# Optimization experiments

Measured on AMD Instinct MI355X. Metric: run time of the kernel, lower is better.

## Reference

```python
import jax, jax.numpy as jnp
import numpy as np

E, N, C, A, S, H, HD, RH = 320000, 20000, 128, 4, 16, 8, 32, 64
AH = H * HD  # 256 attn-head channels; mul_alpha = AH, mul_alpha_head = HD
OUT = 128


def smooth_leaky_relu(x, a=0.2):
    # Equiformer SmoothLeakyReLU: 0.5*((1+a)*x + (1-a)*x*(2*sigmoid(x)-1))
    return 0.5 * ((1 + a) * x + (1 - a) * x * (2.0 * jax.nn.sigmoid(x) - 1.0))


def setup_inputs() -> dict:
    key = jax.random.key(0)
    ks = jax.random.split(key, 20)
    d = {
        'message': jax.random.normal(ks[0], (E, C), jnp.float32),
        'edge_attr': jax.random.normal(ks[1], (E, A), jnp.float32),
        'edge_scalars': jax.random.normal(ks[2], (E, S), jnp.float32),
        'w_rad1': jax.random.normal(ks[3], (S, RH), jnp.float32) / np.sqrt(S),
        'b_rad1': jnp.zeros((RH,), jnp.float32),
        'w_rad2': jax.random.normal(ks[4], (RH, C * A), jnp.float32) / np.sqrt(RH),
        'b_rad2': jnp.zeros((C * A,), jnp.float32),
        'w_dtp_v': jax.random.normal(ks[5], (C, A), jnp.float32) / np.sqrt(A),
        'w_lin_act': jax.random.normal(ks[6], (C, C), jnp.float32) / np.sqrt(C),
        'b_lin_act': jnp.zeros((C,), jnp.float32),
        'w_alpha': jax.random.normal(ks[7], (C, AH), jnp.float32) / np.sqrt(C),
        'b_alpha': jnp.zeros((AH,), jnp.float32),
        'w_lin_v': jax.random.normal(ks[8], (C, AH), jnp.float32) / np.sqrt(C),
        'b_lin_v': jnp.zeros((AH,), jnp.float32),
        'alpha_dot': jax.random.normal(ks[9], (H, HD), jnp.float32) / np.sqrt(HD),
        'w_proj': jax.random.normal(ks[10], (AH, OUT), jnp.float32) / np.sqrt(AH),
        'b_proj': jnp.zeros((OUT,), jnp.float32),
        'edge_dst': jax.random.randint(ks[11], (E,), 0, N, jnp.int32),
        'n_nodes_dst': N,
    }
    return d


def reference(message, edge_attr, edge_scalars,
              w_rad1, b_rad1, w_rad2, b_rad2,
              w_dtp_v, w_lin_act, b_lin_act,
              w_alpha, b_alpha, w_lin_v, b_lin_v,
              alpha_dot, w_proj, b_proj,
              edge_dst, n_nodes_dst):
    n = n_nodes_dst
    # dtp_rad: radial MLP -> per-edge depthwise TP weights [E, C, A]
    h = jax.nn.silu(edge_scalars @ w_rad1 + b_rad1)
    w = (h @ w_rad2 + b_rad2).reshape(-1, C, A)
    # sep_act.dtp (scalar irreps): out[e,c] = msg[e,c] * sum_a w[e,c,a]*attr[e,a]
    msg = message * jnp.einsum('eca,ea->ec', w, edge_attr)
    # sep_alpha -> alpha heads [E, H, HD]
    alpha = (msg @ w_alpha + b_alpha).reshape(-1, H, HD)
    # sep_act.lin + gate (scalars -> SiLU)
    value = jax.nn.silu(msg @ w_lin_act + b_lin_act)
    # sep_value: internal-weight dtp then linear, reshape to heads
    value = value * jnp.einsum('ca,ea->ec', w_dtp_v, edge_attr)
    value = (value @ w_lin_v + b_lin_v).reshape(-1, H, HD)
    # attention logits
    alpha = smooth_leaky_relu(alpha)
    alpha = jnp.einsum('ehk,hk->eh', alpha, alpha_dot)
    # scatter softmax over destination nodes
    amax = jax.ops.segment_max(alpha, edge_dst, num_segments=n)  # [N, H]
    amax = jnp.where(jnp.isfinite(amax), amax, 0.0)
    ex = jnp.exp(alpha - amax[edge_dst])
    denom = jax.ops.segment_sum(ex, edge_dst, num_segments=n)
    alpha = ex / (denom[edge_dst] + 1e-16)
    # weighted scatter-add aggregation
    attn = value * alpha[..., None]  # [E, H, HD]
    node = jax.ops.segment_sum(attn, edge_dst, num_segments=n)  # [N, H, HD]
    node = node.reshape(n, AH)  # heads2vec
    return node @ w_proj + b_proj
```

## Files before the change

### kernel.cpp

```cpp
#include <hip/hip_runtime.h>
#include <hip/hip_bf16.h>

#define C_   128
#define A_   4
#define S_   16
#define RH_  64
#define H_   8
#define AH_  256
#define OUT_ 128

typedef __attribute__((ext_vector_type(8))) short bf16x8;
typedef __attribute__((ext_vector_type(4))) float f32x4;

__device__ __forceinline__ float sigf(float x) { return 1.0f / (1.0f + __expf(-x)); }

__device__ __forceinline__ unsigned short f2bf(float x) {
    unsigned u = __float_as_uint(x);
    unsigned r = (u + 0x7fffu + ((u >> 16) & 1u)) >> 16;
    return (unsigned short)r;
}
__device__ __forceinline__ float bf2f(unsigned short v) {
    return __uint_as_float((unsigned)v << 16);
}

__device__ __forceinline__ unsigned pkbf(float a, float b) {
    union { __hip_bfloat162 h; unsigned u; } c;
    c.h = __float22bfloat162_rn(float2{a, b});
    return c.u;
}

__device__ __forceinline__ unsigned enc(float x) {
    unsigned b = __float_as_uint(x);
    return (b & 0x80000000u) ? ~b : (b | 0x80000000u);
}
__device__ __forceinline__ float dec(unsigned u) {
    unsigned b = (u & 0x80000000u) ? (u & 0x7fffffffu) : ~u;
    return __uint_as_float(b);
}

__global__ void k_pack(const float* __restrict__ W, short* __restrict__ out, int K, int N) {
    const int KS = K / 32;
    const int ct = blockIdx.x / KS, ks = blockIdx.x % KS;
    const int l = threadIdx.x, lr = l & 15, lg = l >> 4;
    bf16x8 v;
    #pragma unroll
    for (int j = 0; j < 8; j++)
        v[j] = (short)f2bf(W[(size_t)(ks * 32 + lg * 8 + j) * N + ct * 16 + lr]);
    *(bf16x8*)&out[((size_t)blockIdx.x * 64 + l) * 8] = v;
}

__global__ void k_pack_dtp(const float* __restrict__ W, short* __restrict__ out) {
    const int ct = blockIdx.x >> 3, ks = blockIdx.x & 7;
    const int l = threadIdx.x, lr = l & 15, lg = l >> 4;
    bf16x8 v;
    #pragma unroll
    for (int j = 0; j < 8; j++)
        v[j] = (short)f2bf(W[(size_t)(ks * 8 + lg * 2 + (j >> 2)) * 512 + (ct * 16 + lr) * 4 + (j & 3)]);
    *(bf16x8*)&out[((size_t)blockIdx.x * 64 + l) * 8] = v;
}

__global__ __launch_bounds__(256) void k_hist(
    const int* __restrict__ edge_dst, int* __restrict__ deg, int E)
{
    const int e = blockIdx.x * 256 + threadIdx.x;
    if (e < E) atomicAdd(&deg[edge_dst[e]], 1);
}

__global__ __launch_bounds__(1024) void k_scan(
    const int* __restrict__ deg, int* __restrict__ cursor, int N)
{
    __shared__ int part[1024];
    const int t = threadIdx.x;
    const int per = (N + 1023) / 1024;
    const int i0 = t * per;
    int s = 0;
    for (int i = 0; i < per; i++) { int idx = i0 + i; if (idx < N) s += deg[idx]; }
    part[t] = s;
    __syncthreads();
    for (int off = 1; off < 1024; off <<= 1) {
        int v = (t >= off) ? part[t - off] : 0;
        __syncthreads();
        part[t] += v;
        __syncthreads();
    }
    int excl = (t == 0) ? 0 : part[t - 1];
    for (int i = 0; i < per; i++) {
        int idx = i0 + i;
        if (idx < N) { cursor[idx] = excl; excl += deg[idx]; }
    }
}

__global__ __launch_bounds__(256) void k_fill(
    const int* __restrict__ edge_dst, int* __restrict__ cursor,
    int* __restrict__ sorted, int E)
{
    const int e = blockIdx.x * 256 + threadIdx.x;
    if (e < E) {
        const int pos = atomicAdd(&cursor[edge_dst[e]], 1);
        sorted[pos] = e;
    }
}

__global__ __launch_bounds__(256, 4) void k_msgalpha(
    const float* __restrict__ message, const float* __restrict__ edge_attr,
    const float* __restrict__ edge_scalars,
    const float* __restrict__ w_rad1, const float* __restrict__ b_rad1,
    const short* __restrict__ w_rad2_lin, const float* __restrict__ b_rad2,
    const short* __restrict__ w_alpha_lin, const float* __restrict__ b_alpha,
    const float* __restrict__ alpha_dot, const int* __restrict__ edge_dst,
    short* __restrict__ msg_bf, float* __restrict__ logits, unsigned* __restrict__ amax_u)
{
    __shared__ __align__(16) char smem[25216];
    short* Ap     = (short*)smem;
    short* msg_s  = (short*)(smem + 16384);
    float* w1_s   = (float*)(smem + 16384);
    float* es_s   = (float*)(smem + 16384 + 4096);
    float* attr_s = (float*)(smem + 24576);
    int*   dst_s  = (int*)(smem + 25088);

    const int t = threadIdx.x;
    const long e0 = (long)blockIdx.x * 32;

    *(float4*)&w1_s[t * 4] = *(const float4*)&w_rad1[t * 4];
    if (t < 128) {
        const int r = t >> 2, s4 = (t & 3) * 4;
        *(float4*)&es_s[r * 17 + s4] = *(const float4*)&edge_scalars[(e0 + r) * S_ + s4];
    }
    if (t < 32) {
        *(float4*)&attr_s[t * 4] = *(const float4*)&edge_attr[(e0 + t) * A_];
        dst_s[t] = edge_dst[e0 + t];
    }
    __syncthreads();

    {
        const int r = t & 31, o0 = (t >> 5) * 8;
        float acc[8];
        #pragma unroll
        for (int i = 0; i < 8; i++) acc[i] = b_rad1[o0 + i];
        #pragma unroll
        for (int s = 0; s < S_; s++) {
            const float ev = es_s[r * 17 + s];
            #pragma unroll
            for (int i = 0; i < 8; i++) acc[i] += ev * w1_s[s * 64 + o0 + i];
        }
        float h[8];
        #pragma unroll
        for (int i = 0; i < 8; i++) { const float x = acc[i]; h[i] = x * sigf(x); }
        const float4 a4 = *(const float4*)&attr_s[r * 4];
        char* base = (char*)Ap + r * 512;
        const int sw = (r & 31) << 4;
        #pragma unroll
        for (int c = 0; c < 4; c++) {
            const float h0 = h[2 * c], h1 = h[2 * c + 1];
            uint4 v;
            v.x = pkbf(h0 * a4.x, h0 * a4.y);
            v.y = pkbf(h0 * a4.z, h0 * a4.w);
            v.z = pkbf(h1 * a4.x, h1 * a4.y);
            v.w = pkbf(h1 * a4.z, h1 * a4.w);
            *(uint4*)(base + ((o0 * 8 + c * 16) ^ sw)) = v;
        }
    }
    __syncthreads();

    const int w = t >> 6, l = t & 63, lr = l & 15, lg = l >> 4;

    {
        #pragma unroll
        for (int q = 0; q < 2; q++) {
            const int ct = w * 2 + q;
            bf16x8 bf[8];
            #pragma unroll
            for (int ks = 0; ks < 8; ks++)
                bf[ks] = *(const bf16x8*)&w_rad2_lin[((size_t)(ct * 8 + ks) * 64 + l) * 8];
            const int col = ct * 16 + lr;
            const float4 b2 = *(const float4*)&b_rad2[col * 4];
            #pragma unroll
            for (int rt = 0; rt < 2; rt++) {
                const int arow = rt * 16 + lr;
                const char* abase = (char*)Ap + arow * 512;
                const int asw = (arow & 31) << 4;
                bf16x8 af[8];
                #pragma unroll
                for (int ks = 0; ks < 8; ks++)
                    af[ks] = *(const bf16x8*)(abase + ((ks * 64 + lg * 16) ^ asw));
                f32x4 acc = {0.f, 0.f, 0.f, 0.f};
                #pragma unroll
                for (int ks = 0; ks < 8; ks++)
                    acc = __builtin_amdgcn_mfma_f32_16x16x32_bf16(af[ks], bf[ks], acc, 0, 0, 0);
                #pragma unroll
                for (int r = 0; r < 4; r++) {
                    const int row = rt * 16 + lg * 4 + r;
                    const float4 a4 = *(const float4*)&attr_s[row * 4];
                    const float badj = a4.x * b2.x + a4.y * b2.y + a4.z * b2.z + a4.w * b2.w;
                    const float m = message[(e0 + row) * C_ + col];
                    *(short*)((char*)msg_s + row * 256 + ((col * 2) ^ ((row & 15) << 4))) =
                        (short)f2bf(m * (acc[r] + badj));
                }
            }
        }
    }
    __syncthreads();

    {
        #pragma unroll
        for (int i = 0; i < 2; i++) {
            const int q = t + i * 256;
            const int row = q >> 4, ch = q & 15;
            const uint4 v = *(const uint4*)((char*)msg_s + row * 256 + ((ch * 16) ^ ((row & 15) << 4)));
            *(uint4*)((char*)msg_bf + ((e0 + row) * 256 + ch * 16)) = v;
        }
    }

    {
        #pragma unroll
        for (int hq = 0; hq < 2; hq++) {
            const int hd = w * 2 + hq;
            bf16x8 waf[2][4];
            float4 ba4[2], ad4[2];
            #pragma unroll
            for (int q = 0; q < 2; q++) {
                const int ctw = hd * 2 + q;
                #pragma unroll
                for (int ks = 0; ks < 4; ks++)
                    waf[q][ks] = *(const bf16x8*)&w_alpha_lin[((size_t)(ctw * 4 + ks) * 64 + l) * 8];
                ba4[q] = *(const float4*)&b_alpha[ctw * 16 + lg * 4];
                ad4[q] = *(const float4*)&alpha_dot[ctw * 16 + lg * 4];
            }
            #pragma unroll
            for (int ct = 0; ct < 2; ct++) {
                const int erow = ct * 16 + lr;
                const char* mbase = (char*)msg_s + erow * 256;
                const int msw = (erow & 15) << 4;
                bf16x8 mb[4];
                #pragma unroll
                for (int ks = 0; ks < 4; ks++)
                    mb[ks] = *(const bf16x8*)(mbase + ((ks * 64 + lg * 16) ^ msw));
                float s = 0.f;
                #pragma unroll
                for (int q = 0; q < 2; q++) {
                    f32x4 acc = {0.f, 0.f, 0.f, 0.f};
                    #pragma unroll
                    for (int ks = 0; ks < 4; ks++)
                        acc = __builtin_amdgcn_mfma_f32_16x16x32_bf16(waf[q][ks], mb[ks], acc, 0, 0, 0);
                    #pragma unroll
                    for (int r = 0; r < 4; r++) {
                        const float x = acc[r] + ((const float*)&ba4[q])[r];
                        const float y = x * (0.2f + 0.8f * sigf(x));
                        s += y * ((const float*)&ad4[q])[r];
                    }
                }
                s += __shfl_xor(s, 16);
                s += __shfl_xor(s, 32);
                if (lg == 0) {
                    const long e = e0 + ct * 16 + lr;
                    logits[e * H_ + hd] = s;
                    atomicMax(&amax_u[dst_s[ct * 16 + lr] * H_ + hd], enc(s));
                }
            }
        }
    }
}

__global__ __launch_bounds__(256) void k_denom(
    const float* __restrict__ logits, const int* __restrict__ edge_dst,
    const int* __restrict__ sorted, const unsigned* __restrict__ amax_u,
    float* __restrict__ denom, int E)
{
    const int idx = blockIdx.x * 256 + threadIdx.x;
    if (idx >= E) return;
    const int g = idx >> 3, h = idx & 7;
    int nprev = -1; float run = 0.f, am = 0.f;
    #pragma unroll 1
    for (int e = 0; e < 8; e++) {
        const int eid = sorted[g * 8 + e];
        const int n = edge_dst[eid];
        if (n != nprev) {
            if (nprev >= 0) atomicAdd(&denom[nprev * H_ + h], run);
            nprev = n; run = 0.f;
            am = dec(amax_u[n * H_ + h]);
        }
        run += __expf(logits[(size_t)eid * H_ + h] - am);
    }
    atomicAdd(&denom[nprev * H_ + h], run);
}

__global__ __launch_bounds__(256, 5) void k_value(
    const short* __restrict__ msg_bf, const float* __restrict__ edge_attr,
    const short* __restrict__ w_lin_act_lin, const float* __restrict__ b_lin_act,
    const float* __restrict__ w_dtp_v,
    const short* __restrict__ w_lin_v_lin, const float* __restrict__ b_lin_v,
    const float* __restrict__ logits, const int* __restrict__ edge_dst,
    const unsigned* __restrict__ amax_u, const float* __restrict__ denom,
    const int* __restrict__ sorted, float* __restrict__ node)
{
    __shared__ __align__(16) char pool[16896];
    __shared__ float attr_s[32][4];
    __shared__ float wgt_s[32][H_];
    __shared__ int   dst_s[32];
    __shared__ int   eid_s[32];
    short* a_s  = (short*)pool;
    short* v_s  = (short*)(pool + 8192);
    short* val2 = (short*)pool;

    const int t = threadIdx.x;
    const int b0 = blockIdx.x * 32;

    if (t < 32) {
        const int e = sorted[b0 + t];
        eid_s[t] = e;
        dst_s[t] = edge_dst[e];
        *(float4*)&attr_s[t][0] = *(const float4*)&edge_attr[(long)e * A_];
    }
    __syncthreads();
    #pragma unroll
    for (int i = 0; i < 2; i++) {
        const int q = t + i * 256;
        const int row = q >> 4, ch = q & 15;
        const uint4 v = *(const uint4*)((const char*)msg_bf + ((long)eid_s[row] * 256 + ch * 16));
        *(uint4*)((char*)a_s + row * 256 + ((ch * 16) ^ ((row & 15) << 4))) = v;
    }
    {
        const int el = t >> 3, h = t & 7;
        const long e = eid_s[el];
        const int n = dst_s[el];
        const float am = dec(amax_u[n * H_ + h]);
        const float d  = denom[n * H_ + h];
        wgt_s[el][h] = __expf(logits[e * H_ + h] - am) / (d + 1e-16f);
    }
    __syncthreads();

    const int w = t >> 6, l = t & 63, lr = l & 15, lg = l >> 4;
    {
        bf16x8 af[2][4];
        #pragma unroll
        for (int rt = 0; rt < 2; rt++)
            #pragma unroll
            for (int ks = 0; ks < 4; ks++) {
                const int arow = rt * 16 + lr;
                af[rt][ks] = *(bf16x8*)((char*)a_s + arow * 256 + ((ks * 64 + lg * 16) ^ ((arow & 15) << 4)));
            }
        #pragma unroll
        for (int q = 0; q < 2; q++) {
            const int ct = w * 2 + q;
            bf16x8 bfg[4];
            #pragma unroll
            for (int ks = 0; ks < 4; ks++)
                bfg[ks] = *(const bf16x8*)&w_lin_act_lin[((size_t)(ct * 4 + ks) * 64 + l) * 8];
            const int col = ct * 16 + lr;
            const float bb = b_lin_act[col];
            const float4 wv = *(const float4*)&w_dtp_v[col * 4];
            #pragma unroll
            for (int rt = 0; rt < 2; rt++) {
                f32x4 acc = {0.f, 0.f, 0.f, 0.f};
                #pragma unroll
                for (int ks = 0; ks < 4; ks++)
                    acc = __builtin_amdgcn_mfma_f32_16x16x32_bf16(af[rt][ks], bfg[ks], acc, 0, 0, 0);
                #pragma unroll
                for (int r = 0; r < 4; r++) {
                    const int row = rt * 16 + lg * 4 + r;
                    float x = acc[r] + bb;
                    x = x * sigf(x);
                    const float4 a4 = *(const float4*)&attr_s[row][0];
                    const float dv = wv.x * a4.x + wv.y * a4.y + wv.z * a4.z + wv.w * a4.w;
                    *(short*)((char*)v_s + row * 256 + ((col * 2) ^ ((row & 15) << 4))) =
                        (short)f2bf(x * dv);
                }
            }
        }
    }
    __syncthreads();

    bf16x8 vf[2][4];
    #pragma unroll
    for (int rt = 0; rt < 2; rt++)
        #pragma unroll
        for (int ks = 0; ks < 4; ks++) {
            const int row = rt * 16 + lr;
            vf[rt][ks] = *(bf16x8*)((char*)v_s + row * 256 + ((ks * 64 + lg * 16) ^ ((row & 15) << 4)));
        }
    __syncthreads();

    #pragma unroll
    for (int q = 0; q < 4; q++) {
        const int ct = w * 4 + q;
        bf16x8 bf[4];
        #pragma unroll
        for (int ks = 0; ks < 4; ks++)
            bf[ks] = *(const bf16x8*)&w_lin_v_lin[((size_t)(ct * 4 + ks) * 64 + l) * 8];
        const int col = ct * 16 + lr;
        const float bb = b_lin_v[col];
        #pragma unroll
        for (int rt = 0; rt < 2; rt++) {
            f32x4 acc = {0.f, 0.f, 0.f, 0.f};
            #pragma unroll
            for (int ks = 0; ks < 4; ks++)
                acc = __builtin_amdgcn_mfma_f32_16x16x32_bf16(vf[rt][ks], bf[ks], acc, 0, 0, 0);
            #pragma unroll
            for (int r = 0; r < 4; r++) {
                const int row = rt * 16 + lg * 4 + r;
                val2[row * 264 + col] = (short)f2bf((acc[r] + bb) * wgt_s[row][col >> 5]);
            }
        }
    }
    __syncthreads();
    {
        const int c = t;
        float run = 0.f;
        int s = 0;
        #pragma unroll 1
        for (int e = 0; e < 32; e++) {
            run += bf2f((unsigned short)val2[e * 264 + c]);
            const bool end = (e == 31) || (dst_s[e + 1] != dst_s[e]);
            if (end) {
                float* np = node + (long)dst_s[e] * AH_ + c;
                if (s == 0 || e == 31) atomicAdd(np, run);
                else *np = run;
                run = 0.f; s = e + 1;
            }
        }
    }
}

__global__ __launch_bounds__(256) void k_proj(
    const float* __restrict__ node, const float* __restrict__ w_proj,
    const float* __restrict__ b_proj, float* __restrict__ out)
{
    __shared__ float node_s[32][AH_];
    const int t = threadIdx.x;
    const long n0 = (long)blockIdx.x * 32;
    #pragma unroll
    for (int i = 0; i < 8; i++) {
        const int idx = t + i * 256;
        const int nl = idx >> 6, c4 = (idx & 63) * 4;
        *(float4*)&node_s[nl][c4] = *(const float4*)&node[(n0 + nl) * AH_ + c4];
    }
    __syncthreads();
    const int j0 = (t & 31) * 4;
    const int g  = t >> 5;
    float4 acc4[4];
    const float4 b = *(const float4*)&b_proj[j0];
    #pragma unroll
    for (int i = 0; i < 4; i++) acc4[i] = b;
    const float* wp = w_proj + j0;
    for (int c4 = 0; c4 < 64; c4++) {
        const float4 w0 = *(const float4*)&wp[(c4 * 4 + 0) * OUT_];
        const float4 w1 = *(const float4*)&wp[(c4 * 4 + 1) * OUT_];
        const float4 w2 = *(const float4*)&wp[(c4 * 4 + 2) * OUT_];
        const float4 w3 = *(const float4*)&wp[(c4 * 4 + 3) * OUT_];
        #pragma unroll
        for (int i = 0; i < 4; i++) {
            const float4 nv = *(const float4*)&node_s[g * 4 + i][c4 * 4];
            acc4[i].x += nv.x * w0.x + nv.y * w1.x + nv.z * w2.x + nv.w * w3.x;
            acc4[i].y += nv.x * w0.y + nv.y * w1.y + nv.z * w2.y + nv.w * w3.y;
            acc4[i].z += nv.x * w0.z + nv.y * w1.z + nv.z * w2.z + nv.w * w3.z;
            acc4[i].w += nv.x * w0.w + nv.y * w1.w + nv.z * w2.w + nv.w * w3.w;
        }
    }
    #pragma unroll
    for (int i = 0; i < 4; i++) {
        const long n = n0 + g * 4 + i;
        *(float4*)&out[n * OUT_ + j0] = acc4[i];
    }
}

extern "C" void kernel_launch(void* const* d_in, const int* in_sizes, int n_in,
                              void* d_out, int out_size, void* d_ws, size_t ws_size,
                              hipStream_t stream)
{
    const float* message      = (const float*)d_in[0];
    const float* edge_attr    = (const float*)d_in[1];
    const float* edge_scalars = (const float*)d_in[2];
    const float* w_rad1       = (const float*)d_in[3];
    const float* b_rad1       = (const float*)d_in[4];
    const float* w_rad2       = (const float*)d_in[5];
    const float* b_rad2       = (const float*)d_in[6];
    const float* w_dtp_v      = (const float*)d_in[7];
    const float* w_lin_act    = (const float*)d_in[8];
    const float* b_lin_act    = (const float*)d_in[9];
    const float* w_alpha      = (const float*)d_in[10];
    const float* b_alpha      = (const float*)d_in[11];
    const float* w_lin_v      = (const float*)d_in[12];
    const float* b_lin_v      = (const float*)d_in[13];
    const float* alpha_dot    = (const float*)d_in[14];
    const float* w_proj       = (const float*)d_in[15];
    const float* b_proj       = (const float*)d_in[16];
    const int*   edge_dst     = (const int*)d_in[17];

    const int E = in_sizes[0] / C_;
    const int N = out_size / OUT_;

    char* ws = (char*)d_ws;
    float*    node     = (float*)ws;
    unsigned* amax_u   = (unsigned*)(node + (size_t)N * AH_);
    float*    denom    = (float*)(amax_u + (size_t)N * H_);
    int*      deg      = (int*)(denom + (size_t)N * H_);
    int*      cursor   = deg + N;
    int*      sorted   = cursor + N;
    short*    w_rad2_l = (short*)(sorted + E);
    short*    w_alph_l = w_rad2_l + 64 * 512;
    short*    w_lact_l = w_alph_l + 128 * 256;
    short*    w_linv_l = w_lact_l + 128 * 128;
    short*    msg_bf   = w_linv_l + 128 * 256;
    float*    logits   = (float*)(msg_bf + (size_t)E * C_);

    hipMemsetAsync(d_ws, 0, (size_t)N * (AH_ + 2 * H_ + 1) * 4, stream);

    const int nbE256 = (E + 255) / 256;
    k_pack_dtp<<<64, 64, 0, stream>>>(w_rad2, w_rad2_l);
    k_pack<<<(256/16)*(128/32), 64, 0, stream>>>(w_alpha,   w_alph_l, 128, 256);
    k_pack<<<(128/16)*(128/32), 64, 0, stream>>>(w_lin_act, w_lact_l, 128, 128);
    k_pack<<<(256/16)*(128/32), 64, 0, stream>>>(w_lin_v,   w_linv_l, 128, 256);
    k_hist<<<nbE256, 256, 0, stream>>>(edge_dst, deg, E);
    k_scan<<<1, 1024, 0, stream>>>(deg, cursor, N);
    k_fill<<<nbE256, 256, 0, stream>>>(edge_dst, cursor, sorted, E);
    k_msgalpha<<<E / 32, 256, 0, stream>>>(message, edge_attr, edge_scalars,
                                           w_rad1, b_rad1, w_rad2_l, b_rad2,
                                           w_alph_l, b_alpha, alpha_dot, edge_dst,
                                           msg_bf, logits, amax_u);
    k_denom<<<nbE256, 256, 0, stream>>>(logits, edge_dst, sorted, amax_u, denom, E);
    k_value<<<E / 32, 256, 0, stream>>>(msg_bf, edge_attr, w_lact_l, b_lin_act, w_dtp_v,
                                        w_linv_l, b_lin_v, logits, edge_dst, amax_u, denom,
                                        sorted, node);
    k_proj<<<N / 32, 256, 0, stream>>>(node, w_proj, b_proj, (float*)d_out);
}
```

Baseline: 403.0 us.

## Double k_msgalpha tile to 64 edges with 512 threads, one column/head per wave

Restructures k_msgalpha so each block processes 64 edges with 8 waves instead of 32 edges with 4. Each wave now owns one radial-weight column tile and one attention head, loading its weight fragments once and reusing them across four row tiles instead of two. This halves the number of blocks and the per-block reloads of weight fragments. The cost is a doubled LDS footprint and launch bounds of (512,4), which could limit occupancy or raise register pressure.

```diff
diff --git a/kernel.cpp b/kernel.cpp
--- a/kernel.cpp
+++ b/kernel.cpp
@@ -101,7 +101,7 @@
     }
 }
 
-__global__ __launch_bounds__(256, 4) void k_msgalpha(
+__global__ __launch_bounds__(512, 4) void k_msgalpha(
     const float* __restrict__ message, const float* __restrict__ edge_attr,
     const float* __restrict__ edge_scalars,
     const float* __restrict__ w_rad1, const float* __restrict__ b_rad1,
@@ -110,30 +110,31 @@
     const float* __restrict__ alpha_dot, const int* __restrict__ edge_dst,
     short* __restrict__ msg_bf, float* __restrict__ logits, unsigned* __restrict__ amax_u)
 {
-    __shared__ __align__(16) char smem[25216];
+    __shared__ __align__(16) char smem[50432];
     short* Ap     = (short*)smem;
-    short* msg_s  = (short*)(smem + 16384);
-    float* w1_s   = (float*)(smem + 16384);
-    float* es_s   = (float*)(smem + 16384 + 4096);
-    float* attr_s = (float*)(smem + 24576);
-    int*   dst_s  = (int*)(smem + 25088);
+    short* msg_s  = (short*)(smem + 32768);
+    float* w1_s   = (float*)(smem + 32768);
+    float* es_s   = (float*)(smem + 32768 + 4096);
+    float* attr_s = (float*)(smem + 49152);
+    int*   dst_s  = (int*)(smem + 50176);
 
     const int t = threadIdx.x;
-    const long e0 = (long)blockIdx.x * 32;
-
-    *(float4*)&w1_s[t * 4] = *(const float4*)&w_rad1[t * 4];
-    if (t < 128) {
-        const int r = t >> 2, s4 = (t & 3) * 4;
+    const long e0 = (long)blockIdx.x * 64;
+
+    if (t < 256) {
+        *(float4*)&w1_s[t * 4] = *(const float4*)&w_rad1[t * 4];
+    } else {
+        const int i = t - 256, r = i >> 2, s4 = (i & 3) * 4;
         *(float4*)&es_s[r * 17 + s4] = *(const float4*)&edge_scalars[(e0 + r) * S_ + s4];
     }
-    if (t < 32) {
+    if (t < 64) {
         *(float4*)&attr_s[t * 4] = *(const float4*)&edge_attr[(e0 + t) * A_];
         dst_s[t] = edge_dst[e0 + t];
     }
     __syncthreads();
 
     {
-        const int r = t & 31, o0 = (t >> 5) * 8;
+        const int r = t & 63, o0 = (t >> 6) * 8;
         float acc[8];
         #pragma unroll
         for (int i = 0; i < 8; i++) acc[i] = b_rad1[o0 + i];
@@ -165,37 +166,33 @@
     const int w = t >> 6, l = t & 63, lr = l & 15, lg = l >> 4;
 
     {
-        #pragma unroll
-        for (int q = 0; q < 2; q++) {
-            const int ct = w * 2 + q;
-            bf16x8 bf[8];
+        bf16x8 bf[8];
+        #pragma unroll
+        for (int ks = 0; ks < 8; ks++)
+            bf[ks] = *(const bf16x8*)&w_rad2_lin[((size_t)(w * 8 + ks) * 64 + l) * 8];
+        const int col = w * 16 + lr;
+        const float4 b2 = *(const float4*)&b_rad2[col * 4];
+        #pragma unroll 1
+        for (int rt = 0; rt < 4; rt++) {
+            const int arow = rt * 16 + lr;
+            const char* abase = (char*)Ap + arow * 512;
+            const int asw = (arow & 31) << 4;
+            bf16x8 af[8];
             #pragma unroll
             for (int ks = 0; ks < 8; ks++)
-                bf[ks] = *(const bf16x8*)&w_rad2_lin[((size_t)(ct * 8 + ks) * 64 + l) * 8];
-            const int col = ct * 16 + lr;
-            const float4 b2 = *(const float4*)&b_rad2[col * 4];
-            #pragma unroll
-            for (int rt = 0; rt < 2; rt++) {
-                const int arow = rt * 16 + lr;
-                const char* abase = (char*)Ap + arow * 512;
-                const int asw = (arow & 31) << 4;
-                bf16x8 af[8];
-                #pragma unroll
-                for (int ks = 0; ks < 8; ks++)
-                    af[ks] = *(const bf16x8*)(abase + ((ks * 64 + lg * 16) ^ asw));
-                f32x4 acc = {0.f, 0.f, 0.f, 0.f};
-                #pragma unroll
-                for (int ks = 0; ks < 8; ks++)
-                    acc = __builtin_amdgcn_mfma_f32_16x16x32_bf16(af[ks], bf[ks], acc, 0, 0, 0);
-                #pragma unroll
-                for (int r = 0; r < 4; r++) {
-                    const int row = rt * 16 + lg * 4 + r;
-                    const float4 a4 = *(const float4*)&attr_s[row * 4];
-                    const float badj = a4.x * b2.x + a4.y * b2.y + a4.z * b2.z + a4.w * b2.w;
-                    const float m = message[(e0 + row) * C_ + col];
-                    *(short*)((char*)msg_s + row * 256 + ((col * 2) ^ ((row & 15) << 4))) =
-                        (short)f2bf(m * (acc[r] + badj));
-                }
+                af[ks] = *(const bf16x8*)(abase + ((ks * 64 + lg * 16) ^ asw));
+            f32x4 acc = {0.f, 0.f, 0.f, 0.f};
+            #pragma unroll
+            for (int ks = 0; ks < 8; ks++)
+                acc = __builtin_amdgcn_mfma_f32_16x16x32_bf16(af[ks], bf[ks], acc, 0, 0, 0);
+            #pragma unroll
+            for (int r = 0; r < 4; r++) {
+                const int row = rt * 16 + lg * 4 + r;
+                const float4 a4 = *(const float4*)&attr_s[row * 4];
+                const float badj = a4.x * b2.x + a4.y * b2.y + a4.z * b2.z + a4.w * b2.w;
+                const float m = message[(e0 + row) * C_ + col];
+                *(short*)((char*)msg_s + row * 256 + ((col * 2) ^ ((row & 15) << 4))) =
+                    (short)f2bf(m * (acc[r] + badj));
             }
         }
     }
@@ -204,7 +201,7 @@
     {
         #pragma unroll
         for (int i = 0; i < 2; i++) {
-            const int q = t + i * 256;
+            const int q = t + i * 512;
             const int row = q >> 4, ch = q & 15;
             const uint4 v = *(const uint4*)((char*)msg_s + row * 256 + ((ch * 16) ^ ((row & 15) << 4)));
             *(uint4*)((char*)msg_bf + ((e0 + row) * 256 + ch * 16)) = v;
@@ -212,50 +209,46 @@
     }
 
     {
-        #pragma unroll
-        for (int hq = 0; hq < 2; hq++) {
-            const int hd = w * 2 + hq;
-            bf16x8 waf[2][4];
-            float4 ba4[2], ad4[2];
+        bf16x8 waf[2][4];
+        float4 ba4[2], ad4[2];
+        #pragma unroll
+        for (int q = 0; q < 2; q++) {
+            const int rt = w * 2 + q;
+            #pragma unroll
+            for (int ks = 0; ks < 4; ks++)
+                waf[q][ks] = *(const bf16x8*)&w_alpha_lin[((size_t)(rt * 4 + ks) * 64 + l) * 8];
+            ba4[q] = *(const float4*)&b_alpha[rt * 16 + lg * 4];
+            ad4[q] = *(const float4*)&alpha_dot[rt * 16 + lg * 4];
+        }
+        #pragma unroll 1
+        for (int ct = 0; ct < 4; ct++) {
+            const int erow = ct * 16 + lr;
+            const char* mbase = (char*)msg_s + erow * 256;
+            const int msw = (erow & 15) << 4;
+            bf16x8 mb[4];
+            #pragma unroll
+            for (int ks = 0; ks < 4; ks++)
+                mb[ks] = *(const bf16x8*)(mbase + ((ks * 64 + lg * 16) ^ msw));
+            float s = 0.f;
             #pragma unroll
             for (int q = 0; q < 2; q++) {
-                const int ctw = hd * 2 + q;
+                f32x4 acc = {0.f, 0.f, 0.f, 0.f};
                 #pragma unroll
                 for (int ks = 0; ks < 4; ks++)
-                    waf[q][ks] = *(const bf16x8*)&w_alpha_lin[((size_t)(ctw * 4 + ks) * 64 + l) * 8];
-                ba4[q] = *(const float4*)&b_alpha[ctw * 16 + lg * 4];
-                ad4[q] = *(const float4*)&alpha_dot[ctw * 16 + lg * 4];
-            }
-            #pragma unroll
-            for (int ct = 0; ct < 2; ct++) {
-                const int erow = ct * 16 + lr;
-                const char* mbase = (char*)msg_s + erow * 256;
-                const int msw = (erow & 15) << 4;
-                bf16x8 mb[4];
+                    acc = __builtin_amdgcn_mfma_f32_16x16x32_bf16(waf[q][ks], mb[ks], acc, 0, 0, 0);
                 #pragma unroll
-                for (int ks = 0; ks < 4; ks++)
-                    mb[ks] = *(const bf16x8*)(mbase + ((ks * 64 + lg * 16) ^ msw));
-                float s = 0.f;
-                #pragma unroll
-                for (int q = 0; q < 2; q++) {
-                    f32x4 acc = {0.f, 0.f, 0.f, 0.f};
-                    #pragma unroll
-                    for (int ks = 0; ks < 4; ks++)
-                        acc = __builtin_amdgcn_mfma_f32_16x16x32_bf16(waf[q][ks], mb[ks], acc, 0, 0, 0);
-                    #pragma unroll
-                    for (int r = 0; r < 4; r++) {
-                        const float x = acc[r] + ((const float*)&ba4[q])[r];
-                        const float y = x * (0.2f + 0.8f * sigf(x));
-                        s += y * ((const float*)&ad4[q])[r];
-                    }
+                for (int r = 0; r < 4; r++) {
+                    const float x = acc[r] + ((const float*)&ba4[q])[r];
+                    const float y = x * (0.2f + 0.8f * sigf(x));
+                    s += y * ((const float*)&ad4[q])[r];
                 }
-                s += __shfl_xor(s, 16);
-                s += __shfl_xor(s, 32);
-                if (lg == 0) {
-                    const long e = e0 + ct * 16 + lr;
-                    logits[e * H_ + hd] = s;
-                    atomicMax(&amax_u[dst_s[ct * 16 + lr] * H_ + hd], enc(s));
-                }
+            }
+            s += __shfl_xor(s, 16);
+            s += __shfl_xor(s, 32);
+            if (lg == 0) {
+                const long e = e0 + ct * 16 + lr;
+                logits[e * H_ + w] = s;
+                atomicMax(&amax_u[dst_s[ct * 16 + lr] * H_ + w], enc(s));
             }
         }
     }
@@ -513,7 +506,7 @@
     k_hist<<<nbE256, 256, 0, stream>>>(edge_dst, deg, E);
     k_scan<<<1, 1024, 0, stream>>>(deg, cursor, N);
     k_fill<<<nbE256, 256, 0, stream>>>(edge_dst, cursor, sorted, E);
-    k_msgalpha<<<E / 32, 256, 0, stream>>>(message, edge_attr, edge_scalars,
+    k_msgalpha<<<E / 64, 512, 0, stream>>>(message, edge_attr, edge_scalars,
                                            w_rad1, b_rad1, w_rad2_l, b_rad2,
                                            w_alph_l, b_alpha, alpha_dot, edge_dst,
                                            msg_bf, logits, amax_u);
```

After: 397.5 us. Within noise of the previous version (-1.4%).
